# Performance work log

Hardware: AMD Instinct MI355X
Metric: run time of the kernel (lower is better)

The kernel has to match this reference:

```python
import jax, jax.numpy as jnp
import numpy as np

B, C, H, W = 32, 256, 32, 32
NUM_EMB = 1024
BETA = 0.25  # commitment_loss_weight


def setup_inputs() -> dict:
    key = jax.random.key(0)
    k_u, k_cb = jax.random.split(key)
    u = jax.random.normal(k_u, (B, C, H, W), dtype=jnp.float32)
    # kaiming_normal_ fan_in, relu: std = sqrt(2 / fan_in), fan_in = embedding_dim
    cb_std = float(np.sqrt(2.0 / C))
    codebook = jax.random.normal(k_cb, (NUM_EMB, C), dtype=jnp.float32) * cb_std
    return {"u": u, "codebook": codebook}


def reference(u, codebook):
    # u: [B, C, H, W] -> flat: [B*H*W, C]
    flat = jnp.transpose(u, (0, 2, 3, 1)).reshape(-1, C)
    # squared euclidean distances (argmin-equivalent to torch.cdist)
    d = (
        jnp.sum(flat * flat, axis=1, keepdims=True)
        - 2.0 * flat @ codebook.T
        + jnp.sum(codebook * codebook, axis=1)[None, :]
    )  # [B*H*W, NUM_EMB]
    encoding_indices = jnp.argmin(d, axis=1)  # [B*H*W]
    z_q = codebook[encoding_indices].reshape(B, H, W, C)
    z_q = jnp.transpose(z_q, (0, 3, 1, 2))  # [B, C, H, W]
    # straight-through (note: z_q is NOT detached here, matching the source)
    z_train = z_q + (u - jax.lax.stop_gradient(u))
    codebook_loss = jnp.mean((z_q - jax.lax.stop_gradient(u)) ** 2)
    commitment_loss = jnp.mean((u - jax.lax.stop_gradient(z_q)) ** 2)
    vq_loss = codebook_loss + BETA * commitment_loss
    return u, z_train, vq_loss, encoding_indices.reshape(B, H, W)
```

## Files before the change

### kernel.cpp

```cpp
#include <hip/hip_runtime.h>
#include <hip/hip_bf16.h>

#define BATCH 32
#define CHN   256
#define HWSZ  1024
#define NPIX  32768
#define NEMB  1024
#define NELEM 8388608
#define FLT_BIG 3.402823466e+38f

#define WS_CBT   0
#define WS_CNORM 262144
#define WS_XNORM 263168
#define WS_ACCUM 295936

#define OUT_U    0
#define OUT_ZT   8388608
#define OUT_LOSS 16777216
#define OUT_IDX  16777217

__global__ __launch_bounds__(256) void k_prep_cb(const float* __restrict__ cb,
                                                 float* __restrict__ ws) {
    int n = blockIdx.x;
    int c = threadIdx.x;
    float v = cb[(size_t)n * CHN + c];
    ws[WS_CBT + (size_t)c * NEMB + n] = v;
    float s = v * v;
    #pragma unroll
    for (int off = 32; off > 0; off >>= 1) s += __shfl_down(s, off, 64);
    __shared__ float ls[4];
    int w = threadIdx.x >> 6;
    if ((threadIdx.x & 63) == 0) ls[w] = s;
    __syncthreads();
    if (threadIdx.x == 0) ws[WS_CNORM + n] = (ls[0] + ls[1]) + (ls[2] + ls[3]);
}

__global__ __launch_bounds__(256) void k_prep_x(const float* __restrict__ u,
                                                float* __restrict__ ws) {
    int P0   = blockIdx.x * 64;
    int b    = P0 / HWSZ;
    int hw0  = P0 % HWSZ;
    int lane = threadIdx.x & 63;
    int grp  = threadIdx.x >> 6;
    const float* up = u + (size_t)b * CHN * HWSZ + hw0 + lane;
    float s = 0.f;
    int cbase = grp * 64;
    #pragma unroll 8
    for (int c = 0; c < 64; ++c) {
        float v = up[(size_t)(cbase + c) * HWSZ];
        s = fmaf(v, v, s);
    }
    __shared__ float ls[4][64];
    ls[grp][lane] = s;
    __syncthreads();
    if (grp == 0) {
        float x = (ls[0][lane] + ls[1][lane]) + (ls[2][lane] + ls[3][lane]);
        ws[WS_XNORM + P0 + lane] = x;
    }
    if (blockIdx.x == 0 && threadIdx.x == 0)
        *(double*)&ws[WS_ACCUM] = 0.0;
}

__global__ __launch_bounds__(256, 2) void k_argmin(const float* __restrict__ u,
                                                   const float* __restrict__ ws,
                                                   float* __restrict__ out_idx) {
    __shared__ float s_u[32][64];
    __shared__ float s_cb[32][256];

    const float* cbT   = ws + WS_CBT;
    const float* cnorm = ws + WS_CNORM;
    const float* xnorm = ws + WS_XNORM;

    int T   = blockIdx.x;
    int P0  = T * 64;
    int b   = P0 / HWSZ;
    int hw0 = P0 % HWSZ;
    int tid = threadIdx.x;
    int tx  = tid & 7;
    int ty  = tid >> 3;

    const float* ub = u + (size_t)b * CHN * HWSZ + hw0;

    float xn[8];
    #pragma unroll
    for (int i = 0; i < 8; ++i) xn[i] = xnorm[P0 + tx * 8 + i];

    float dmin[8];
    int   imin[8];
    #pragma unroll
    for (int i = 0; i < 8; ++i) { dmin[i] = FLT_BIG; imin[i] = 0; }

    for (int nt = 0; nt < 4; ++nt) {
        int n0 = nt * 256;
        float acc[8][8];
        #pragma unroll
        for (int i = 0; i < 8; ++i)
            #pragma unroll
            for (int j = 0; j < 8; ++j) acc[i][j] = 0.f;

        for (int kc = 0; kc < 8; ++kc) {
            int c0 = kc * 32;
            __syncthreads();
            #pragma unroll
            for (int it = 0; it < 2; ++it) {
                int q   = it * 256 + tid;
                int k   = q >> 4;
                int pix = (q & 15) << 2;
                float4 v = *(const float4*)&ub[(size_t)(c0 + k) * HWSZ + pix];
                *(float4*)&s_u[k][pix] = v;
            }
            #pragma unroll
            for (int it = 0; it < 8; ++it) {
                int q = it * 256 + tid;
                int k = q >> 6;
                int j = (q & 63) << 2;
                float4 v = *(const float4*)&cbT[(size_t)(c0 + k) * NEMB + n0 + j];
                *(float4*)&s_cb[k][j] = v;
            }
            __syncthreads();
            #pragma unroll 4
            for (int k = 0; k < 32; ++k) {
                float4 a0 = *(const float4*)&s_u[k][tx * 8];
                float4 a1 = *(const float4*)&s_u[k][tx * 8 + 4];
                float4 b0 = *(const float4*)&s_cb[k][ty * 8];
                float4 b1 = *(const float4*)&s_cb[k][ty * 8 + 4];
                float a[8]; float bb[8];
                a[0]=a0.x; a[1]=a0.y; a[2]=a0.z; a[3]=a0.w;
                a[4]=a1.x; a[5]=a1.y; a[6]=a1.z; a[7]=a1.w;
                bb[0]=b0.x; bb[1]=b0.y; bb[2]=b0.z; bb[3]=b0.w;
                bb[4]=b1.x; bb[5]=b1.y; bb[6]=b1.z; bb[7]=b1.w;
                #pragma unroll
                for (int i = 0; i < 8; ++i)
                    #pragma unroll
                    for (int j = 0; j < 8; ++j)
                        acc[i][j] = fmaf(a[i], bb[j], acc[i][j]);
            }
        }
        float cn[8];
        #pragma unroll
        for (int j = 0; j < 8; ++j) cn[j] = cnorm[n0 + ty * 8 + j];
        #pragma unroll
        for (int i = 0; i < 8; ++i) {
            #pragma unroll
            for (int j = 0; j < 8; ++j) {
                float t1 = xn[i] - 2.0f * acc[i][j];
                float d  = t1 + cn[j];
                int   n  = n0 + ty * 8 + j;
                if (d < dmin[i]) { dmin[i] = d; imin[i] = n; }
            }
        }
    }

    __syncthreads();
    float* red_d = &s_cb[0][0];
    int*   red_i = (int*)&s_cb[8][0];
    #pragma unroll
    for (int i = 0; i < 8; ++i) {
        red_d[(tx * 8 + i) * 32 + ty] = dmin[i];
        red_i[(tx * 8 + i) * 32 + ty] = imin[i];
    }
    __syncthreads();
    if (tid < 64) {
        float bd = FLT_BIG; int bi = 0x7fffffff;
        #pragma unroll
        for (int t = 0; t < 32; ++t) {
            float d = red_d[tid * 32 + t];
            int   n = red_i[tid * 32 + t];
            if (d < bd || (d == bd && n < bi)) { bd = d; bi = n; }
        }
        out_idx[P0 + tid] = (float)bi;
    }
}

__global__ __launch_bounds__(256) void k_out(const float* __restrict__ u,
                                             const float* __restrict__ cb,
                                             const float* __restrict__ idxf,
                                             float* __restrict__ out,
                                             double* __restrict__ accum) {
    int P0   = blockIdx.x * 64;
    int b    = P0 / HWSZ;
    int hw0  = P0 % HWSZ;
    int lane = threadIdx.x & 63;
    int grp  = threadIdx.x >> 6;
    int p    = P0 + lane;
    int idx  = (int)idxf[p];
    const float* ub    = u + (size_t)b * CHN * HWSZ + hw0 + lane;
    float*       o0    = out + OUT_U  + (size_t)b * CHN * HWSZ + hw0 + lane;
    float*       o1    = out + OUT_ZT + (size_t)b * CHN * HWSZ + hw0 + lane;
    const float* cbrow = cb + (size_t)idx * CHN;
    float s = 0.f;
    #pragma unroll
    for (int r = 0; r < 8; ++r) {
        int c0 = grp * 8 + r * 32;
        float4 z0 = *(const float4*)&cbrow[c0];
        float4 z1 = *(const float4*)&cbrow[c0 + 4];
        float zq[8];
        zq[0]=z0.x; zq[1]=z0.y; zq[2]=z0.z; zq[3]=z0.w;
        zq[4]=z1.x; zq[5]=z1.y; zq[6]=z1.z; zq[7]=z1.w;
        #pragma unroll
        for (int cc = 0; cc < 8; ++cc) {
            int c = c0 + cc;
            float uv = ub[(size_t)c * HWSZ];
            float zv = zq[cc];
            o0[(size_t)c * HWSZ] = uv;
            o1[(size_t)c * HWSZ] = zv;
            float df = zv - uv;
            s = fmaf(df, df, s);
        }
    }
    #pragma unroll
    for (int off = 32; off > 0; off >>= 1) s += __shfl_down(s, off, 64);
    __shared__ float ls[4];
    if (lane == 0) ls[grp] = s;
    __syncthreads();
    if (threadIdx.x == 0) {
        float tot = (ls[0] + ls[1]) + (ls[2] + ls[3]);
        atomicAdd(accum, (double)tot);
    }
}

__global__ void k_loss(const double* __restrict__ accum,
                       float* __restrict__ out_loss) {
    float m = (float)(*accum / (double)NELEM);
    out_loss[0] = m + 0.25f * m;
}

extern "C" void kernel_launch(void* const* d_in, const int* in_sizes, int n_in,
                              void* d_out, int out_size, void* d_ws, size_t ws_size,
                              hipStream_t stream) {
    const float* u  = (const float*)d_in[0];
    const float* cb = (const float*)d_in[1];
    float* out = (float*)d_out;
    float* ws  = (float*)d_ws;

    k_prep_cb<<<dim3(NEMB),      dim3(256), 0, stream>>>(cb, ws);
    k_prep_x <<<dim3(NPIX / 64), dim3(256), 0, stream>>>(u, ws);
    k_argmin <<<dim3(NPIX / 64), dim3(256), 0, stream>>>(u, ws, out + OUT_IDX);
    k_out    <<<dim3(NPIX / 64), dim3(256), 0, stream>>>(u, cb, out + OUT_IDX, out,
                                                         (double*)(ws + WS_ACCUM));
    k_loss   <<<dim3(1),         dim3(1),   0, stream>>>((const double*)(ws + WS_ACCUM),
                                                         out + OUT_LOSS);
}
```

Measured before the change: 333.5 us.

## Double-buffer argmin tiles with async global-to-LDS loads

The distance/argmin kernel now keeps two shared-memory buffers for the input and codebook tiles. It issues the next tile's loads with direct global-to-LDS instructions (global_load_lds) while computing on the current tile, so there is one barrier per stage instead of two. The aim is to hide global load latency behind the FMA loop and to skip the register round-trip on the way into shared memory. In exchange, LDS use per block doubles to about 80KB, which still fits two blocks per CU. Correctness relies on the barrier waiting for the outstanding async loads.

```diff
diff --git a/kernel.cpp b/kernel.cpp
--- a/kernel.cpp
+++ b/kernel.cpp
@@ -18,6 +18,12 @@
 #define OUT_ZT   8388608
 #define OUT_LOSS 16777216
 #define OUT_IDX  16777217
+
+__device__ __forceinline__ void gld_lds16(const float* g, float* lds) {
+    __builtin_amdgcn_global_load_lds(
+        (const __attribute__((address_space(1))) void*)g,
+        (__attribute__((address_space(3))) void*)lds, 16, 0, 0);
+}
 
 __global__ __launch_bounds__(256) void k_prep_cb(const float* __restrict__ cb,
                                                  float* __restrict__ ws) {
@@ -64,8 +70,8 @@
 __global__ __launch_bounds__(256, 2) void k_argmin(const float* __restrict__ u,
                                                    const float* __restrict__ ws,
                                                    float* __restrict__ out_idx) {
-    __shared__ float s_u[32][64];
-    __shared__ float s_cb[32][256];
+    __shared__ float s_u[2][32][64];
+    __shared__ float s_cb[2][32][256];
 
     const float* cbT   = ws + WS_CBT;
     const float* cnorm = ws + WS_CNORM;
@@ -81,6 +87,13 @@
 
     const float* ub = u + (size_t)b * CHN * HWSZ + hw0;
 
+    int uq0_k  = tid >> 4;
+    int uq0_p  = (tid & 15) << 2;
+    int uq1_k  = (256 + tid) >> 4;
+    int uq1_p  = (tid & 15) << 2;
+    int cb_k0  = tid >> 6;
+    int cb_j   = (tid & 63) << 2;
+
     float xn[8];
     #pragma unroll
     for (int i = 0; i < 8; ++i) xn[i] = xnorm[P0 + tx * 8 + i];
@@ -89,6 +102,25 @@
     int   imin[8];
     #pragma unroll
     for (int i = 0; i < 8; ++i) { dmin[i] = FLT_BIG; imin[i] = 0; }
+
+    auto stage = [&](int s, int buf) {
+        int nt = s >> 3;
+        int kc = s & 7;
+        int n0 = nt * 256;
+        int c0 = kc * 32;
+        float* su  = &s_u[buf][0][0];
+        float* scb = &s_cb[buf][0][0];
+        gld_lds16(&ub[(size_t)(c0 + uq0_k) * HWSZ + uq0_p], &su[tid * 4]);
+        gld_lds16(&ub[(size_t)(c0 + uq1_k) * HWSZ + uq1_p], &su[(256 + tid) * 4]);
+        #pragma unroll
+        for (int it = 0; it < 8; ++it) {
+            int k = cb_k0 + it * 4;
+            gld_lds16(&cbT[(size_t)(c0 + k) * NEMB + n0 + cb_j],
+                      &scb[(it * 256 + tid) * 4]);
+        }
+    };
+
+    stage(0, 0);
 
     for (int nt = 0; nt < 4; ++nt) {
         int n0 = nt * 256;
@@ -99,31 +131,18 @@
             for (int j = 0; j < 8; ++j) acc[i][j] = 0.f;
 
         for (int kc = 0; kc < 8; ++kc) {
-            int c0 = kc * 32;
+            int s   = nt * 8 + kc;
+            int buf = s & 1;
             __syncthreads();
-            #pragma unroll
-            for (int it = 0; it < 2; ++it) {
-                int q   = it * 256 + tid;
-                int k   = q >> 4;
-                int pix = (q & 15) << 2;
-                float4 v = *(const float4*)&ub[(size_t)(c0 + k) * HWSZ + pix];
-                *(float4*)&s_u[k][pix] = v;
-            }
-            #pragma unroll
-            for (int it = 0; it < 8; ++it) {
-                int q = it * 256 + tid;
-                int k = q >> 6;
-                int j = (q & 63) << 2;
-                float4 v = *(const float4*)&cbT[(size_t)(c0 + k) * NEMB + n0 + j];
-                *(float4*)&s_cb[k][j] = v;
-            }
-            __syncthreads();
-            #pragma unroll 4
+            if (s < 31) stage(s + 1, buf ^ 1);
+            const float* su  = &s_u[buf][0][0];
+            const float* scb = &s_cb[buf][0][0];
+            #pragma unroll 8
             for (int k = 0; k < 32; ++k) {
-                float4 a0 = *(const float4*)&s_u[k][tx * 8];
-                float4 a1 = *(const float4*)&s_u[k][tx * 8 + 4];
-                float4 b0 = *(const float4*)&s_cb[k][ty * 8];
-                float4 b1 = *(const float4*)&s_cb[k][ty * 8 + 4];
+                float4 a0 = *(const float4*)&su[k * 64 + tx * 8];
+                float4 a1 = *(const float4*)&su[k * 64 + tx * 8 + 4];
+                float4 b0 = *(const float4*)&scb[k * 256 + ty * 8];
+                float4 b1 = *(const float4*)&scb[k * 256 + ty * 8 + 4];
                 float a[8]; float bb[8];
                 a[0]=a0.x; a[1]=a0.y; a[2]=a0.z; a[3]=a0.w;
                 a[4]=a1.x; a[5]=a1.y; a[6]=a1.z; a[7]=a1.w;
@@ -152,8 +171,8 @@
     }
 
     __syncthreads();
-    float* red_d = &s_cb[0][0];
-    int*   red_i = (int*)&s_cb[8][0];
+    float* red_d = &s_cb[0][0][0];
+    int*   red_i = (int*)&s_cb[0][8][0];
     #pragma unroll
     for (int i = 0; i < 8; ++i) {
         red_d[(tx * 8 + i) * 32 + ty] = dmin[i];
```

Result: faster. 326.3 us (-2.2%).
